# Kernel tuning notes

Hardware: AMD Instinct MI355X
Metric: run time of the kernel (lower is better)

The kernel has to match this reference:

```python
import jax, jax.numpy as jnp
import numpy as np

TOPK = 2
RENORMALIZE = True

T, H, I, E = 2048, 2048, 5632, 8  # tokens, hidden, intermediate, experts


def setup_inputs() -> dict:
    key = jax.random.key(0)
    k1, k2, k3, k4 = jax.random.split(key, 4)
    x = jax.random.normal(k1, (T, H), dtype=jnp.float32)
    gating_output = jax.random.normal(k2, (T, E), dtype=jnp.float32)
    # gate_up_proj: concat of gate [E,I,H] and up [E,I,H] along dim 1 -> [E,2I,H]
    w1 = jax.random.normal(k3, (E, 2 * I, H), dtype=jnp.float32) * 0.02
    # down_proj: [E, H, I]
    w2 = jax.random.normal(k4, (E, H, I), dtype=jnp.float32) * 0.02
    return {"x": x, "gating_output": gating_output, "w1": w1, "w2": w2}


def _route(gating_output):
    # standard (non-grouped) top-k softmax routing, renormalized
    probs = jax.nn.softmax(gating_output, axis=-1)            # [T, E]
    topk_w, topk_idx = jax.lax.top_k(probs, TOPK)             # [T, K]
    if RENORMALIZE:
        topk_w = topk_w / jnp.sum(topk_w, axis=-1, keepdims=True)
    t = gating_output.shape[0]
    route = jnp.zeros((t, gating_output.shape[1]), dtype=topk_w.dtype)
    route = route.at[jnp.arange(t)[:, None], topk_idx].set(topk_w)  # [T, E]
    return route


def reference(x, gating_output, w1, w2):
    route = _route(gating_output)                             # [T, E]
    inter = w2.shape[-1]
    out = jnp.zeros_like(x)
    # loop over small fixed expert count; each iter is dense GEMM work
    for e in range(w1.shape[0]):
        gu = x @ w1[e].T                                      # [T, 2I]
        h = jax.nn.silu(gu[:, :inter]) * gu[:, inter:]        # SwiGLU  [T, I]
        out = out + (h @ w2[e].T) * route[:, e:e + 1]         # [T, H]
    return out
```

## Files before the change

kernel.cpp:

```cpp
#include <hip/hip_runtime.h>
#include <hip/hip_bf16.h>


#define TT 2048
#define HH 2048
#define II 5632
#define NE 8

using f32x4  = __attribute__((ext_vector_type(4))) float;
using bf16x8 = __attribute__((ext_vector_type(8))) short;

__device__ __forceinline__ uint32_t bfbits(float f) {
    __hip_bfloat16 h = __float2bfloat16(f);
    unsigned short u;
    __builtin_memcpy(&u, &h, 2);
    return (uint32_t)u;
}
__device__ __forceinline__ uint32_t pk2(float a, float b) {
    return bfbits(a) | (bfbits(b) << 16);
}
__device__ __forceinline__ uint4 pk8(const float4& a, const float4& b) {
    uint4 r;
    r.x = pk2(a.x, a.y); r.y = pk2(a.z, a.w);
    r.z = pk2(b.x, b.y); r.w = pk2(b.z, b.w);
    return r;
}
__device__ __forceinline__ void gl16(const void* g, void* l) {
    __builtin_amdgcn_global_load_lds(
        (const __attribute__((address_space(1))) unsigned int*)g,
        (__attribute__((address_space(3))) unsigned int*)l, 16, 0, 0);
}

__global__ void cvt_x(const float* __restrict__ x, __hip_bfloat16* __restrict__ xb) {
    const int i = (blockIdx.x * 256 + threadIdx.x) * 8;
    float4 a = *(const float4*)(x + i);
    float4 b = *(const float4*)(x + i + 4);
    *(uint4*)(xb + i) = pk8(a, b);
}

__global__ void route_topk(const float* __restrict__ gating,
                           int* __restrict__ tk_idx, float* __restrict__ tk_w) {
    int t = blockIdx.x * 256 + threadIdx.x;
    if (t >= TT) return;
    float g[NE];
#pragma unroll
    for (int e = 0; e < NE; e++) g[e] = gating[t * NE + e];
    int i0 = 0; float b0 = g[0];
#pragma unroll
    for (int e = 1; e < NE; e++) if (g[e] > b0) { b0 = g[e]; i0 = e; }
    int i1 = (i0 == 0) ? 1 : 0; float b1 = g[i1];
#pragma unroll
    for (int e = 0; e < NE; e++) if (e != i0 && g[e] > b1) { b1 = g[e]; i1 = e; }
    float ex = expf(b1 - b0);
    float w0 = 1.f / (1.f + ex);
    float w1 = ex / (1.f + ex);
    tk_idx[2 * t] = i0; tk_idx[2 * t + 1] = i1;
    tk_w[2 * t] = w0;  tk_w[2 * t + 1] = w1;
}

__global__ void build_lists(const int* __restrict__ tk_idx, const float* __restrict__ tk_w,
                            int* __restrict__ list_tok, float* __restrict__ list_w,
                            int* __restrict__ counts) {
    const int e = blockIdx.x;
    const int tid = threadIdx.x;
    int flag[8]; float wt[8];
    int cnt = 0;
#pragma unroll
    for (int j = 0; j < 8; j++) {
        int t = tid * 8 + j;
        int f = -1;
        if (tk_idx[2 * t] == e) f = 0;
        else if (tk_idx[2 * t + 1] == e) f = 1;
        flag[j] = f;
        wt[j] = (f >= 0) ? tk_w[2 * t + f] : 0.f;
        cnt += (f >= 0) ? 1 : 0;
    }
    __shared__ int s[256];
    s[tid] = cnt;
    __syncthreads();
    for (int d = 1; d < 256; d <<= 1) {
        int v = (tid >= d) ? s[tid - d] : 0;
        __syncthreads();
        s[tid] += v;
        __syncthreads();
    }
    int pos = s[tid] - cnt;
#pragma unroll
    for (int j = 0; j < 8; j++) {
        if (flag[j] >= 0) {
            list_tok[e * TT + pos] = tid * 8 + j;
            list_w[e * TT + pos] = wt[j];
            pos++;
        }
    }
    if (tid == 255) counts[e] = s[255];
}

__global__ __launch_bounds__(256, 4) void gemm1_swiglu(
    const __hip_bfloat16* __restrict__ xb, const float* __restrict__ w1,
    const int* __restrict__ list_tok, const int* __restrict__ counts,
    __hip_bfloat16* __restrict__ hbuf) {
    const int e = blockIdx.y >> 4;
    const int mt = blockIdx.y & 15;
    const int cnt = counts[e];
    const int row0 = mt * 128;
    if (row0 >= cnt) return;
    int off = 0;
#pragma unroll
    for (int i = 0; i < NE; i++) if (i < e) off += counts[i];
    const int valid = min(128, cnt - row0);
    const int n0 = blockIdx.x * 64;
    const int tid = threadIdx.x;
    const int w = tid >> 6, l = tid & 63;

    __shared__ uint4 As[2 * 512];
    __shared__ uint4 Bg[2][256];
    __shared__ uint4 Bu[2][256];

    const char *aSrc0, *aSrc1;
    {
        int r0 = w * 16 + (l >> 2);
        int r1 = r0 + 64;
        int t0 = list_tok[e * TT + row0 + min(r0, valid - 1)];
        int t1 = list_tok[e * TT + row0 + min(r1, valid - 1)];
        int s0 = (l & 3) ^ ((r0 >> 1) & 3);
        int s1 = (l & 3) ^ ((r1 >> 1) & 3);
        aSrc0 = (const char*)(xb + (size_t)t0 * HH + s0 * 8);
        aSrc1 = (const char*)(xb + (size_t)t1 * HH + s1 * 8);
    }
    auto STAGEA = [&](int kt, int b) {
        char* ab = (char*)As + b * 8192 + w * 1024;
        gl16(aSrc0 + (size_t)kt * 64, ab);
        gl16(aSrc1 + (size_t)kt * 64, ab + 4096);
    };

    const int br = tid >> 2, bu2 = tid & 3;
    const float* gS = w1 + (size_t)e * (2 * II) * HH + (size_t)(n0 + br) * HH + bu2 * 8;
    const float* uS = gS + (size_t)II * HH;
    const int bwi = br * 4 + (bu2 ^ ((br >> 1) & 3));

    float4 rGa, rGb, rUa, rUb;
    auto LOADB = [&](int kt) {
        const int k = kt * 32;
        rGa = *(const float4*)(gS + k); rGb = *(const float4*)(gS + k + 4);
        rUa = *(const float4*)(uS + k); rUb = *(const float4*)(uS + k + 4);
    };
    auto STOREB = [&](int b) {
        Bg[b][bwi] = pk8(rGa, rGb);
        Bu[b][bwi] = pk8(rUa, rUb);
    };

    const int wm = w >> 1, wn = w & 1;
    const int l15 = l & 15, ks = l >> 4;
    int aidx[4], bidx[2];
#pragma unroll
    for (int m = 0; m < 4; m++) { int r = wm * 64 + m * 16 + l15; aidx[m] = r * 4 + (ks ^ ((r >> 1) & 3)); }
#pragma unroll
    for (int n = 0; n < 2; n++) { int c = wn * 32 + n * 16 + l15; bidx[n] = c * 4 + (ks ^ ((c >> 1) & 3)); }

    f32x4 accg[4][2], accu[4][2];
#pragma unroll
    for (int m = 0; m < 4; m++)
#pragma unroll
        for (int n = 0; n < 2; n++) { accg[m][n] = 0; accu[m][n] = 0; }

    STAGEA(0, 0); LOADB(0); STOREB(0);
    __syncthreads();
    const int KT = HH / 32;
#pragma unroll 2
    for (int kt = 0; kt < KT; ++kt) {
        const int cur = kt & 1;
        if (kt + 1 < KT) {
            STAGEA(kt + 1, cur ^ 1);
            LOADB(kt + 1);
        }
        bf16x8 af[4], gf[2], uf[2];
        const uint4* Ab = As + cur * 512;
#pragma unroll
        for (int m = 0; m < 4; m++) { uint4 t = Ab[aidx[m]]; af[m] = __builtin_bit_cast(bf16x8, t); }
#pragma unroll
        for (int n = 0; n < 2; n++) {
            uint4 t = Bg[cur][bidx[n]]; gf[n] = __builtin_bit_cast(bf16x8, t);
            uint4 t2 = Bu[cur][bidx[n]]; uf[n] = __builtin_bit_cast(bf16x8, t2);
        }
#pragma unroll
        for (int m = 0; m < 4; m++)
#pragma unroll
            for (int n = 0; n < 2; n++) {
                accg[m][n] = __builtin_amdgcn_mfma_f32_16x16x32_bf16(af[m], gf[n], accg[m][n], 0, 0, 0);
                accu[m][n] = __builtin_amdgcn_mfma_f32_16x16x32_bf16(af[m], uf[n], accu[m][n], 0, 0, 0);
            }
        if (kt + 1 < KT) STOREB(cur ^ 1);
        __syncthreads();
    }

#pragma unroll
    for (int m = 0; m < 4; m++) {
#pragma unroll
        for (int r = 0; r < 4; r++) {
            const int lr = wm * 64 + m * 16 + ks * 4 + r;
            if (lr < valid) {
                __hip_bfloat16* hrow = hbuf + (size_t)(off + row0 + lr) * II;
#pragma unroll
                for (int n = 0; n < 2; n++) {
                    const int col = n0 + wn * 32 + n * 16 + l15;
                    float g = accg[m][n][r], u = accu[m][n][r];
                    float h = g / (1.f + __expf(-g)) * u;
                    hrow[col] = __float2bfloat16(h);
                }
            }
        }
    }
}

__global__ __launch_bounds__(512, 4) void gemm2_scatter(
    const __hip_bfloat16* __restrict__ hbuf, const float* __restrict__ w2,
    const int* __restrict__ list_tok, const float* __restrict__ list_w,
    const int* __restrict__ counts, float* __restrict__ out) {
    const int e = blockIdx.y >> 4;
    const int mt = blockIdx.y & 15;
    const int cnt = counts[e];
    const int row0 = mt * 128;
    if (row0 >= cnt) return;
    int off = 0;
#pragma unroll
    for (int i = 0; i < NE; i++) if (i < e) off += counts[i];
    const int valid = min(128, cnt - row0);
    const int n0 = blockIdx.x * 128;
    const int tid = threadIdx.x;
    const int w = tid >> 6, l = tid & 63;

    __shared__ uint4 As[2 * 512];
    __shared__ uint4 Bs[2][512];

    const char* aSrc;
    {
        int r = w * 16 + (l >> 2);
        int s = (l & 3) ^ ((r >> 1) & 3);
        aSrc = (const char*)(hbuf + (size_t)(off + row0 + min(r, valid - 1)) * II + s * 8);
    }
    auto STAGEA = [&](int kt, int b) {
        char* ab = (char*)As + b * 8192 + w * 1024;
        gl16(aSrc + (size_t)kt * 64, ab);
    };

    const int br = tid >> 2, bu2 = tid & 3;
    const float* bS = w2 + (size_t)e * HH * II + (size_t)(n0 + br) * II + bu2 * 8;
    const int bwi = br * 4 + (bu2 ^ ((br >> 1) & 3));

    float4 rBa, rBb;
    auto LOADB = [&](int kt) {
        const int k = kt * 32;
        rBa = *(const float4*)(bS + k); rBb = *(const float4*)(bS + k + 4);
    };
    auto STOREB = [&](int b) {
        Bs[b][bwi] = pk8(rBa, rBb);
    };

    const int wm = w >> 2, wn = w & 3;
    const int l15 = l & 15, ks = l >> 4;
    int aidx[4], bidx[2];
#pragma unroll
    for (int m = 0; m < 4; m++) { int r = wm * 64 + m * 16 + l15; aidx[m] = r * 4 + (ks ^ ((r >> 1) & 3)); }
#pragma unroll
    for (int n = 0; n < 2; n++) { int c = wn * 32 + n * 16 + l15; bidx[n] = c * 4 + (ks ^ ((c >> 1) & 3)); }

    f32x4 acc[4][2];
#pragma unroll
    for (int m = 0; m < 4; m++)
#pragma unroll
        for (int n = 0; n < 2; n++) acc[m][n] = 0;

    STAGEA(0, 0); LOADB(0); STOREB(0);
    __syncthreads();
    const int KT = II / 32;
#pragma unroll 2
    for (int kt = 0; kt < KT; ++kt) {
        const int cur = kt & 1;
        if (kt + 1 < KT) {
            STAGEA(kt + 1, cur ^ 1);
            LOADB(kt + 1);
        }
        bf16x8 af[4], bf[2];
        const uint4* Ab = As + cur * 512;
#pragma unroll
        for (int m = 0; m < 4; m++) { uint4 t = Ab[aidx[m]]; af[m] = __builtin_bit_cast(bf16x8, t); }
#pragma unroll
        for (int n = 0; n < 2; n++) { uint4 t = Bs[cur][bidx[n]]; bf[n] = __builtin_bit_cast(bf16x8, t); }
#pragma unroll
        for (int m = 0; m < 4; m++)
#pragma unroll
            for (int n = 0; n < 2; n++)
                acc[m][n] = __builtin_amdgcn_mfma_f32_16x16x32_bf16(af[m], bf[n], acc[m][n], 0, 0, 0);
        if (kt + 1 < KT) STOREB(cur ^ 1);
        __syncthreads();
    }

#pragma unroll
    for (int m = 0; m < 4; m++) {
#pragma unroll
        for (int r = 0; r < 4; r++) {
            const int lr = wm * 64 + m * 16 + ks * 4 + r;
            if (lr < valid) {
                const int tok = list_tok[e * TT + row0 + lr];
                const float wt = list_w[e * TT + row0 + lr];
                float* orow = out + (size_t)tok * HH;
#pragma unroll
                for (int n = 0; n < 2; n++) {
                    const int col = n0 + wn * 32 + n * 16 + l15;
                    atomicAdd(orow + col, acc[m][n][r] * wt);
                }
            }
        }
    }
}

extern "C" void kernel_launch(void* const* d_in, const int* in_sizes, int n_in,
                              void* d_out, int out_size, void* d_ws, size_t ws_size,
                              hipStream_t stream) {
    const float* x      = (const float*)d_in[0];
    const float* gating = (const float*)d_in[1];
    const float* w1     = (const float*)d_in[2];
    const float* w2     = (const float*)d_in[3];
    float* out = (float*)d_out;
    char* ws = (char*)d_ws;

    int*   list_tok = (int*)(ws + 0);
    float* list_w   = (float*)(ws + (64 << 10));
    int*   counts   = (int*)(ws + (128 << 10));
    int*   tk_idx   = (int*)(ws + (132 << 10));
    float* tk_w     = (float*)(ws + (148 << 10));
    __hip_bfloat16* hbuf = (__hip_bfloat16*)(ws + (1 << 20));

    __hip_bfloat16* xb = (__hip_bfloat16*)d_out;

    route_topk<<<TT / 256, 256, 0, stream>>>(gating, tk_idx, tk_w);
    build_lists<<<NE, 256, 0, stream>>>(tk_idx, tk_w, list_tok, list_w, counts);
    cvt_x<<<TT * HH / (256 * 8), 256, 0, stream>>>(x, xb);
    gemm1_swiglu<<<dim3(II / 64, NE * 16), 256, 0, stream>>>(xb, w1, list_tok, counts, hbuf);
    (void)hipMemsetAsync(d_out, 0, (size_t)TT * HH * sizeof(float), stream);
    gemm2_scatter<<<dim3(HH / 128, NE * 16), 512, 0, stream>>>(hbuf, w2, list_tok, list_w, counts, out);
}
```

Baseline: 735.4 us.

## Double M-tile to 256 rows in both MoE GEMMs to cut fp32 weight reloads

```diff
diff --git a/kernel.cpp b/kernel.cpp
--- a/kernel.cpp
+++ b/kernel.cpp
@@ -96,31 +96,30 @@
     if (tid == 255) counts[e] = s[255];
 }
 
-__global__ __launch_bounds__(256, 4) void gemm1_swiglu(
+__global__ __launch_bounds__(512, 4) void gemm1_swiglu(
     const __hip_bfloat16* __restrict__ xb, const float* __restrict__ w1,
     const int* __restrict__ list_tok, const int* __restrict__ counts,
     __hip_bfloat16* __restrict__ hbuf) {
-    const int e = blockIdx.y >> 4;
-    const int mt = blockIdx.y & 15;
+    const int e = blockIdx.y >> 3;
+    const int mt = blockIdx.y & 7;
     const int cnt = counts[e];
-    const int row0 = mt * 128;
+    const int row0 = mt * 256;
     if (row0 >= cnt) return;
     int off = 0;
 #pragma unroll
     for (int i = 0; i < NE; i++) if (i < e) off += counts[i];
-    const int valid = min(128, cnt - row0);
+    const int valid = min(256, cnt - row0);
     const int n0 = blockIdx.x * 64;
     const int tid = threadIdx.x;
     const int w = tid >> 6, l = tid & 63;
 
-    __shared__ uint4 As[2 * 512];
-    __shared__ uint4 Bg[2][256];
-    __shared__ uint4 Bu[2][256];
+    __shared__ uint4 As[2 * 1024];
+    __shared__ uint4 Bs[2][512];
 
     const char *aSrc0, *aSrc1;
     {
         int r0 = w * 16 + (l >> 2);
-        int r1 = r0 + 64;
+        int r1 = r0 + 128;
         int t0 = list_tok[e * TT + row0 + min(r0, valid - 1)];
         int t1 = list_tok[e * TT + row0 + min(r1, valid - 1)];
         int s0 = (l & 3) ^ ((r0 >> 1) & 3);
@@ -129,34 +128,39 @@
         aSrc1 = (const char*)(xb + (size_t)t1 * HH + s1 * 8);
     }
     auto STAGEA = [&](int kt, int b) {
-        char* ab = (char*)As + b * 8192 + w * 1024;
+        char* ab = (char*)As + b * 16384 + w * 1024;
         gl16(aSrc0 + (size_t)kt * 64, ab);
-        gl16(aSrc1 + (size_t)kt * 64, ab + 4096);
+        gl16(aSrc1 + (size_t)kt * 64, ab + 8192);
     };
 
     const int br = tid >> 2, bu2 = tid & 3;
-    const float* gS = w1 + (size_t)e * (2 * II) * HH + (size_t)(n0 + br) * HH + bu2 * 8;
-    const float* uS = gS + (size_t)II * HH;
+    const float* bSrc;
+    {
+        const float* base = w1 + (size_t)e * (2 * II) * HH;
+        int r = (br < 64) ? (n0 + br) : (II + n0 + (br - 64));
+        bSrc = base + (size_t)r * HH + bu2 * 8;
+    }
     const int bwi = br * 4 + (bu2 ^ ((br >> 1) & 3));
 
-    float4 rGa, rGb, rUa, rUb;
+    float4 rBa, rBb;
     auto LOADB = [&](int kt) {
         const int k = kt * 32;
-        rGa = *(const float4*)(gS + k); rGb = *(const float4*)(gS + k + 4);
-        rUa = *(const float4*)(uS + k); rUb = *(const float4*)(uS + k + 4);
+        rBa = *(const float4*)(bSrc + k); rBb = *(const float4*)(bSrc + k + 4);
     };
-    auto STOREB = [&](int b) {
-        Bg[b][bwi] = pk8(rGa, rGb);
-        Bu[b][bwi] = pk8(rUa, rUb);
-    };
+    auto STOREB = [&](int b) { Bs[b][bwi] = pk8(rBa, rBb); };
 
     const int wm = w >> 1, wn = w & 1;
     const int l15 = l & 15, ks = l >> 4;
-    int aidx[4], bidx[2];
+    int aidx[4], bgidx[2], buidx[2];
 #pragma unroll
     for (int m = 0; m < 4; m++) { int r = wm * 64 + m * 16 + l15; aidx[m] = r * 4 + (ks ^ ((r >> 1) & 3)); }
 #pragma unroll
-    for (int n = 0; n < 2; n++) { int c = wn * 32 + n * 16 + l15; bidx[n] = c * 4 + (ks ^ ((c >> 1) & 3)); }
+    for (int n = 0; n < 2; n++) {
+        int cg = wn * 32 + n * 16 + l15;
+        int cu = cg + 64;
+        bgidx[n] = cg * 4 + (ks ^ ((cg >> 1) & 3));
+        buidx[n] = cu * 4 + (ks ^ ((cu >> 1) & 3));
+    }
 
     f32x4 accg[4][2], accu[4][2];
 #pragma unroll
@@ -174,22 +178,23 @@
             STAGEA(kt + 1, cur ^ 1);
             LOADB(kt + 1);
         }
-        bf16x8 af[4], gf[2], uf[2];
-        const uint4* Ab = As + cur * 512;
-#pragma unroll
-        for (int m = 0; m < 4; m++) { uint4 t = Ab[aidx[m]]; af[m] = __builtin_bit_cast(bf16x8, t); }
+        bf16x8 gf[2], uf[2];
 #pragma unroll
         for (int n = 0; n < 2; n++) {
-            uint4 t = Bg[cur][bidx[n]]; gf[n] = __builtin_bit_cast(bf16x8, t);
-            uint4 t2 = Bu[cur][bidx[n]]; uf[n] = __builtin_bit_cast(bf16x8, t2);
-        }
-#pragma unroll
-        for (int m = 0; m < 4; m++)
+            uint4 t = Bs[cur][bgidx[n]]; gf[n] = __builtin_bit_cast(bf16x8, t);
+            uint4 t2 = Bs[cur][buidx[n]]; uf[n] = __builtin_bit_cast(bf16x8, t2);
+        }
+        const uint4* Ab = As + cur * 1024;
+#pragma unroll
+        for (int m = 0; m < 4; m++) {
+            uint4 t = Ab[aidx[m]];
+            bf16x8 af = __builtin_bit_cast(bf16x8, t);
 #pragma unroll
             for (int n = 0; n < 2; n++) {
-                accg[m][n] = __builtin_amdgcn_mfma_f32_16x16x32_bf16(af[m], gf[n], accg[m][n], 0, 0, 0);
-                accu[m][n] = __builtin_amdgcn_mfma_f32_16x16x32_bf16(af[m], uf[n], accu[m][n], 0, 0, 0);
+                accg[m][n] = __builtin_amdgcn_mfma_f32_16x16x32_bf16(af, gf[n], accg[m][n], 0, 0, 0);
+                accu[m][n] = __builtin_amdgcn_mfma_f32_16x16x32_bf16(af, uf[n], accu[m][n], 0, 0, 0);
             }
+        }
         if (kt + 1 < KT) STOREB(cur ^ 1);
         __syncthreads();
     }
@@ -217,57 +222,59 @@
     const __hip_bfloat16* __restrict__ hbuf, const float* __restrict__ w2,
     const int* __restrict__ list_tok, const float* __restrict__ list_w,
     const int* __restrict__ counts, float* __restrict__ out) {
-    const int e = blockIdx.y >> 4;
-    const int mt = blockIdx.y & 15;
+    const int e = blockIdx.y >> 3;
+    const int mt = blockIdx.y & 7;
     const int cnt = counts[e];
-    const int row0 = mt * 128;
+    const int row0 = mt * 256;
     if (row0 >= cnt) return;
     int off = 0;
 #pragma unroll
     for (int i = 0; i < NE; i++) if (i < e) off += counts[i];
-    const int valid = min(128, cnt - row0);
+    const int valid = min(256, cnt - row0);
     const int n0 = blockIdx.x * 128;
     const int tid = threadIdx.x;
     const int w = tid >> 6, l = tid & 63;
 
-    __shared__ uint4 As[2 * 512];
+    __shared__ uint4 As[2 * 1024];
     __shared__ uint4 Bs[2][512];
 
-    const char* aSrc;
+    const char *aSrc0, *aSrc1;
     {
-        int r = w * 16 + (l >> 2);
-        int s = (l & 3) ^ ((r >> 1) & 3);
-        aSrc = (const char*)(hbuf + (size_t)(off + row0 + min(r, valid - 1)) * II + s * 8);
+        int r0 = w * 16 + (l >> 2);
+        int r1 = r0 + 128;
+        int s0 = (l & 3) ^ ((r0 >> 1) & 3);
+        int s1 = (l & 3) ^ ((r1 >> 1) & 3);
+        aSrc0 = (const char*)(hbuf + (size_t)(off + row0 + min(r0, valid - 1)) * II + s0 * 8);
+        aSrc1 = (const char*)(hbuf + (size_t)(off + row0 + min(r1, valid - 1)) * II + s1 * 8);
     }
     auto STAGEA = [&](int kt, int b) {
-        char* ab = (char*)As + b * 8192 + w * 1024;
-        gl16(aSrc + (size_t)kt * 64, ab);
+        char* ab = (char*)As + b * 16384 + w * 1024;
+        gl16(aSrc0 + (size_t)kt * 64, ab);
+        gl16(aSrc1 + (size_t)kt * 64, ab + 8192);
     };
 
     const int br = tid >> 2, bu2 = tid & 3;
-    const float* bS = w2 + (size_t)e * HH * II + (size_t)(n0 + br) * II + bu2 * 8;
+    const float* bSrc = w2 + (size_t)e * HH * II + (size_t)(n0 + br) * II + bu2 * 8;
     const int bwi = br * 4 + (bu2 ^ ((br >> 1) & 3));
 
     float4 rBa, rBb;
     auto LOADB = [&](int kt) {
         const int k = kt * 32;
-        rBa = *(const float4*)(bS + k); rBb = *(const float4*)(bS + k + 4);
+        rBa = *(const float4*)(bSrc + k); rBb = *(const float4*)(bSrc + k + 4);
     };
-    auto STOREB = [&](int b) {
-        Bs[b][bwi] = pk8(rBa, rBb);
-    };
+    auto STOREB = [&](int b) { Bs[b][bwi] = pk8(rBa, rBb); };
 
     const int wm = w >> 2, wn = w & 3;
     const int l15 = l & 15, ks = l >> 4;
-    int aidx[4], bidx[2];
-#pragma unroll
-    for (int m = 0; m < 4; m++) { int r = wm * 64 + m * 16 + l15; aidx[m] = r * 4 + (ks ^ ((r >> 1) & 3)); }
+    int aidx[8], bidx[2];
+#pragma unroll
+    for (int m = 0; m < 8; m++) { int r = wm * 128 + m * 16 + l15; aidx[m] = r * 4 + (ks ^ ((r >> 1) & 3)); }
 #pragma unroll
     for (int n = 0; n < 2; n++) { int c = wn * 32 + n * 16 + l15; bidx[n] = c * 4 + (ks ^ ((c >> 1) & 3)); }
 
-    f32x4 acc[4][2];
-#pragma unroll
-    for (int m = 0; m < 4; m++)
+    f32x4 acc[8][2];
+#pragma unroll
+    for (int m = 0; m < 8; m++)
 #pragma unroll
         for (int n = 0; n < 2; n++) acc[m][n] = 0;
 
@@ -281,26 +288,27 @@
             STAGEA(kt + 1, cur ^ 1);
             LOADB(kt + 1);
         }
-        bf16x8 af[4], bf[2];
-        const uint4* Ab = As + cur * 512;
-#pragma unroll
-        for (int m = 0; m < 4; m++) { uint4 t = Ab[aidx[m]]; af[m] = __builtin_bit_cast(bf16x8, t); }
+        bf16x8 bf[2];
 #pragma unroll
         for (int n = 0; n < 2; n++) { uint4 t = Bs[cur][bidx[n]]; bf[n] = __builtin_bit_cast(bf16x8, t); }
-#pragma unroll
-        for (int m = 0; m < 4; m++)
+        const uint4* Ab = As + cur * 1024;
+#pragma unroll
+        for (int m = 0; m < 8; m++) {
+            uint4 t = Ab[aidx[m]];
+            bf16x8 af = __builtin_bit_cast(bf16x8, t);
 #pragma unroll
             for (int n = 0; n < 2; n++)
-                acc[m][n] = __builtin_amdgcn_mfma_f32_16x16x32_bf16(af[m], bf[n], acc[m][n], 0, 0, 0);
+                acc[m][n] = __builtin_amdgcn_mfma_f32_16x16x32_bf16(af, bf[n], acc[m][n], 0, 0, 0);
+        }
         if (kt + 1 < KT) STOREB(cur ^ 1);
         __syncthreads();
     }
 
 #pragma unroll
-    for (int m = 0; m < 4; m++) {
+    for (int m = 0; m < 8; m++) {
 #pragma unroll
         for (int r = 0; r < 4; r++) {
-            const int lr = wm * 64 + m * 16 + ks * 4 + r;
+            const int lr = wm * 128 + m * 16 + ks * 4 + r;
             if (lr < valid) {
                 const int tok = list_tok[e * TT + row0 + lr];
                 const float wt = list_w[e * TT + row0 + lr];
@@ -337,7 +345,7 @@
     route_topk<<<TT / 256, 256, 0, stream>>>(gating, tk_idx, tk_w);
     build_lists<<<NE, 256, 0, stream>>>(tk_idx, tk_w, list_tok, list_w, counts);
     cvt_x<<<TT * HH / (256 * 8), 256, 0, stream>>>(x, xb);
-    gemm1_swiglu<<<dim3(II / 64, NE * 16), 256, 0, stream>>>(xb, w1, list_tok, counts, hbuf);
+    gemm1_swiglu<<<dim3(II / 64, NE * 8), 512, 0, stream>>>(xb, w1, list_tok, counts, hbuf);
     (void)hipMemsetAsync(d_out, 0, (size_t)TT * HH * sizeof(float), stream);
-    gemm2_scatter<<<dim3(HH / 128, NE * 16), 512, 0, stream>>>(hbuf, w2, list_tok, list_w, counts, out);
-}
+    gemm2_scatter<<<dim3(HH / 128, NE * 8), 512, 0, stream>>>(hbuf, w2, list_tok, list_w, counts, out);
+}
```

New measurement: 689.8 us. -6.2%, faster.
